# Performance work log

Measured on AMD Instinct MI355X. Metric: run time of the kernel, lower is better.

The kernel has to match this reference:

```python
import jax, jax.numpy as jnp
import numpy as np

N_ATOMS = 100000
N_EDGES = 1000000
HIDDEN = 64
OUT_DIM = 128
N_LAYERS = 3
N_ELEMENTS = 100


def setup_inputs() -> dict:
    key = jax.random.key(0)
    ks = jax.random.split(key, 14)
    s = 0.05
    return {
        "atomic_numbers": jax.random.randint(ks[0], (N_ATOMS,), 0, N_ELEMENTS),
        "positions": jax.random.normal(ks[1], (N_ATOMS, 3), jnp.float32),
        "lattice": jax.random.normal(ks[2], (3, 3), jnp.float32),
        "edge_index": jax.random.randint(ks[3], (2, N_EDGES), 0, N_ATOMS),
        "emb_table": jax.random.normal(ks[4], (N_ELEMENTS, HIDDEN), jnp.float32) * s,
        "W_lin": jax.random.normal(ks[5], (N_LAYERS, HIDDEN, HIDDEN), jnp.float32) * s,
        "b_lin": jax.random.normal(ks[6], (N_LAYERS, HIDDEN), jnp.float32) * s,
        "W_gate": jax.random.normal(ks[7], (N_LAYERS, 2 * HIDDEN, HIDDEN), jnp.float32) * s,
        "b_gate": jax.random.normal(ks[8], (N_LAYERS, HIDDEN), jnp.float32) * s,
        "W_out1": jax.random.normal(ks[9], (HIDDEN, HIDDEN), jnp.float32) * s,
        "b_out1": jax.random.normal(ks[10], (HIDDEN,), jnp.float32) * s,
        "W_out2": jax.random.normal(ks[11], (HIDDEN, OUT_DIM), jnp.float32) * s,
        "b_out2": jax.random.normal(ks[12], (OUT_DIM,), jnp.float32) * s,
    }


def reference(atomic_numbers, positions, lattice, edge_index,
              emb_table, W_lin, b_lin, W_gate, b_gate,
              W_out1, b_out1, W_out2, b_out2):
    # positions/lattice unused when edge_index is provided (matches original).
    x = emb_table[atomic_numbers]            # [N, H] embedding lookup
    row, col = edge_index[0], edge_index[1]
    n = x.shape[0]
    for i in range(W_lin.shape[0]):          # fixed small layer count
        xn = x[col]                          # [E, H] neighbor gather
        gate_in = jnp.concatenate([x[row], xn], axis=-1)  # [E, 2H]
        gate = jax.nn.sigmoid(gate_in @ W_gate[i] + b_gate[i])
        messages = gate * (xn @ W_lin[i] + b_lin[i])       # [E, H]
        agg = jax.ops.segment_sum(messages, row, num_segments=n)  # scatter-add
        x = jax.nn.relu(agg + x @ W_lin[i] + b_lin[i])
    pooled = x.mean(axis=0)                  # [H] mean pool over atoms
    h = jax.nn.relu(pooled @ W_out1 + b_out1)
    return h @ W_out2 + b_out2               # [OUT_DIM]
```

## Files before the change

### kernel.cpp

```cpp
#include <hip/hip_runtime.h>
#include <hip/hip_bf16.h>
#include <stdint.h>


#define H 64
#define SCAN_BS 256
#define SCAN_ELEMS 1024

typedef __attribute__((ext_vector_type(8))) short bf16x8;
typedef __attribute__((ext_vector_type(4))) float f32x4;

__device__ __forceinline__ float sigmoidf_fast(float z) {
  return __builtin_amdgcn_rcpf(1.f + __expf(-z));
}

__device__ __forceinline__ ushort f2bf(float f) {
  uint32_t u = __float_as_uint(f);
  u = (u + 0x7fffu + ((u >> 16) & 1u)) >> 16;
  return (ushort)u;
}
__device__ __forceinline__ uint32_t pack_gl(float gc, float lin) {
  uint32_t ug = __float_as_uint(gc);
  ug = (ug + 0x7fffu + ((ug >> 16) & 1u)) >> 16;
  uint32_t ul = __float_as_uint(lin);
  ul = ((ul + 0x7fffu + ((ul >> 16) & 1u)) >> 16) << 16;
  return ul | ug;
}
__device__ __forceinline__ float unpack_gc(uint32_t p) {
  return __uint_as_float(p << 16);
}
__device__ __forceinline__ float unpack_lin(uint32_t p) {
  return __uint_as_float(p & 0xffff0000u);
}

__global__ void hist_kernel(const int* __restrict__ row, int* __restrict__ hist,
                            int E) {
  for (int e = blockIdx.x * blockDim.x + threadIdx.x; e < E;
       e += gridDim.x * blockDim.x)
    atomicAdd(&hist[row[e]], 1);
}

__global__ __launch_bounds__(SCAN_BS) void scan_partial_kernel(
    const int* __restrict__ hist, int* __restrict__ bsum, int N) {
  __shared__ int red[SCAN_BS];
  const int tid = threadIdx.x;
  const int base = blockIdx.x * SCAN_ELEMS + tid * 4;
  int s = 0;
  if (base + 3 < N) {
    const int4 v = *(const int4*)(hist + base);
    s = v.x + v.y + v.z + v.w;
  } else {
    for (int j = 0; j < 4; j++) if (base + j < N) s += hist[base + j];
  }
  red[tid] = s;
  __syncthreads();
  for (int off = SCAN_BS / 2; off > 0; off >>= 1) {
    if (tid < off) red[tid] += red[tid + off];
    __syncthreads();
  }
  if (tid == 0) bsum[blockIdx.x] = red[0];
}

__global__ __launch_bounds__(1024) void scan_bsum_kernel(
    const int* __restrict__ bsum, int* __restrict__ boff, int nb) {
  __shared__ int sh[1024];
  const int tid = threadIdx.x;
  const int mine = (tid < nb) ? bsum[tid] : 0;
  sh[tid] = mine;
  __syncthreads();
  for (int off = 1; off < 1024; off <<= 1) {
    const int v = (tid >= off) ? sh[tid - off] : 0;
    __syncthreads();
    sh[tid] += v;
    __syncthreads();
  }
  if (tid < nb) boff[tid] = sh[tid] - mine;
}

__global__ __launch_bounds__(SCAN_BS) void scan_apply_kernel(
    const int* __restrict__ hist, const int* __restrict__ boff,
    int* __restrict__ offs, int* __restrict__ offs_work, int N, int E) {
  __shared__ int red[SCAN_BS];
  const int tid = threadIdx.x;
  const int base = blockIdx.x * SCAN_ELEMS + tid * 4;
  int v0 = 0, v1 = 0, v2 = 0, v3 = 0;
  if (base + 3 < N) {
    const int4 v = *(const int4*)(hist + base);
    v0 = v.x; v1 = v.y; v2 = v.z; v3 = v.w;
  } else {
    if (base < N)     v0 = hist[base];
    if (base + 1 < N) v1 = hist[base + 1];
    if (base + 2 < N) v2 = hist[base + 2];
    if (base + 3 < N) v3 = hist[base + 3];
  }
  const int s = v0 + v1 + v2 + v3;
  red[tid] = s;
  __syncthreads();
  for (int off = 1; off < SCAN_BS; off <<= 1) {
    const int v = (tid >= off) ? red[tid - off] : 0;
    __syncthreads();
    red[tid] += v;
    __syncthreads();
  }
  int run = boff[blockIdx.x] + red[tid] - s;
  if (base < N)     { offs[base] = run;     offs_work[base] = run;     run += v0; }
  if (base + 1 < N) { offs[base + 1] = run; offs_work[base + 1] = run; run += v1; }
  if (base + 2 < N) { offs[base + 2] = run; offs_work[base + 2] = run; run += v2; }
  if (base + 3 < N) { offs[base + 3] = run; offs_work[base + 3] = run; run += v3; }
  if (blockIdx.x == 0 && tid == 0) offs[N] = E;
}

__global__ void scatter_kernel(const int* __restrict__ row,
                               const int* __restrict__ col,
                               int* __restrict__ offs_work,
                               int* __restrict__ cols, int E) {
  for (int e = blockIdx.x * blockDim.x + threadIdx.x; e < E;
       e += gridDim.x * blockDim.x) {
    const int pos = atomicAdd(&offs_work[row[e]], 1);
    cols[pos] = col[e];
  }
}

template <bool FIRST>
__global__ __launch_bounds__(256) void node_mm3_mfma(
    const ushort* __restrict__ x, const int* __restrict__ an,
    const float* __restrict__ emb, const float* __restrict__ Wl,
    const float* __restrict__ bl, const float* __restrict__ Wgr,
    const float* __restrict__ Wgc, const float* __restrict__ bg,
    float* __restrict__ gr, uint32_t* __restrict__ glpk, int N) {
  const int tid = threadIdx.x;
  const int lane = tid & 63, wid = tid >> 6;
  const int l15 = lane & 15, kg = lane >> 4;

  bf16x8 bfrag[3][4][2];
#pragma unroll
  for (int mat = 0; mat < 3; mat++) {
    const float* Wm = (mat == 0) ? Wl : (mat == 1) ? Wgr : Wgc;
#pragma unroll
    for (int nt = 0; nt < 4; nt++) {
#pragma unroll
      for (int ks = 0; ks < 2; ks++) {
        const float* wp = Wm + (size_t)(ks * 32 + kg * 8) * H + nt * 16 + l15;
        bf16x8 b;
#pragma unroll
        for (int j = 0; j < 8; j++) b[j] = (short)f2bf(wp[(size_t)j * H]);
        bfrag[mat][nt][ks] = b;
      }
    }
  }

  const int mbase = blockIdx.x * 64 + wid * 16;
  const int arow = mbase + l15;
  const int arow_c = min(arow, N - 1);

  bf16x8 afrag0, afrag1;
  if (FIRST) {
    const int a = an[arow_c];
    const float* src = emb + (size_t)a * H + kg * 8;
    const float4 u0 = *(const float4*)(src);
    const float4 u1 = *(const float4*)(src + 4);
    const float4 u2 = *(const float4*)(src + 32);
    const float4 u3 = *(const float4*)(src + 36);
    bf16x8 t0, t1;
    t0[0] = (short)f2bf(u0.x); t0[1] = (short)f2bf(u0.y);
    t0[2] = (short)f2bf(u0.z); t0[3] = (short)f2bf(u0.w);
    t0[4] = (short)f2bf(u1.x); t0[5] = (short)f2bf(u1.y);
    t0[6] = (short)f2bf(u1.z); t0[7] = (short)f2bf(u1.w);
    t1[0] = (short)f2bf(u2.x); t1[1] = (short)f2bf(u2.y);
    t1[2] = (short)f2bf(u2.z); t1[3] = (short)f2bf(u2.w);
    t1[4] = (short)f2bf(u3.x); t1[5] = (short)f2bf(u3.y);
    t1[6] = (short)f2bf(u3.z); t1[7] = (short)f2bf(u3.w);
    afrag0 = t0; afrag1 = t1;
  } else {
    const ushort* src = x + (size_t)arow_c * H + kg * 8;
    afrag0 = *(const bf16x8*)(src);
    afrag1 = *(const bf16x8*)(src + 32);
  }

  f32x4 accL[4], accR[4], accC[4];
#pragma unroll
  for (int nt = 0; nt < 4; nt++) {
    const float blv = bl[nt * 16 + l15];
    const float bgv = bg[nt * 16 + l15];
    accL[nt] = (f32x4){blv, blv, blv, blv};
    accR[nt] = (f32x4){0.f, 0.f, 0.f, 0.f};
    accC[nt] = (f32x4){bgv, bgv, bgv, bgv};
  }
#pragma unroll
  for (int nt = 0; nt < 4; nt++) {
    accL[nt] = __builtin_amdgcn_mfma_f32_16x16x32_bf16(afrag0, bfrag[0][nt][0], accL[nt], 0, 0, 0);
    accL[nt] = __builtin_amdgcn_mfma_f32_16x16x32_bf16(afrag1, bfrag[0][nt][1], accL[nt], 0, 0, 0);
    accR[nt] = __builtin_amdgcn_mfma_f32_16x16x32_bf16(afrag0, bfrag[1][nt][0], accR[nt], 0, 0, 0);
    accR[nt] = __builtin_amdgcn_mfma_f32_16x16x32_bf16(afrag1, bfrag[1][nt][1], accR[nt], 0, 0, 0);
    accC[nt] = __builtin_amdgcn_mfma_f32_16x16x32_bf16(afrag0, bfrag[2][nt][0], accC[nt], 0, 0, 0);
    accC[nt] = __builtin_amdgcn_mfma_f32_16x16x32_bf16(afrag1, bfrag[2][nt][1], accC[nt], 0, 0, 0);
  }
#pragma unroll
  for (int nt = 0; nt < 4; nt++) {
#pragma unroll
    for (int r = 0; r < 4; r++) {
      const int atom = mbase + kg * 4 + r;
      if (atom < N) {
        const size_t o = (size_t)atom * H + nt * 16 + l15;
        gr[o] = accR[nt][r];
        glpk[o] = pack_gl(accC[nt][r], accL[nt][r]);
      }
    }
  }
}

__global__ __launch_bounds__(256) void agg_kernel(
    const float* __restrict__ gr, const uint32_t* __restrict__ glpk,
    const int* __restrict__ offs, const int* __restrict__ cols,
    ushort* __restrict__ x, int N) {
  const int lane = threadIdx.x & 63, w = threadIdx.x >> 6;
  for (int i = blockIdx.x * 4 + w; i < N; i += gridDim.x * 4) {
    const int s = offs[i], e = offs[i + 1];
    const float gri = gr[(size_t)i * H + lane];
    float acc = 0.f;
    for (int cb = s; cb < e; cb += 64) {
      const int nchunk = min(64, e - cb);
      const int myc = (lane < nchunk) ? cols[cb + lane] : 0;
      int j = 0;
      for (; j + 3 < nchunk; j += 4) {
        const int c0 = __shfl(myc, j + 0), c1 = __shfl(myc, j + 1);
        const int c2 = __shfl(myc, j + 2), c3 = __shfl(myc, j + 3);
        const uint32_t p0 = glpk[(size_t)c0 * H + lane];
        const uint32_t p1 = glpk[(size_t)c1 * H + lane];
        const uint32_t p2 = glpk[(size_t)c2 * H + lane];
        const uint32_t p3 = glpk[(size_t)c3 * H + lane];
        acc += unpack_lin(p0) * sigmoidf_fast(gri + unpack_gc(p0));
        acc += unpack_lin(p1) * sigmoidf_fast(gri + unpack_gc(p1));
        acc += unpack_lin(p2) * sigmoidf_fast(gri + unpack_gc(p2));
        acc += unpack_lin(p3) * sigmoidf_fast(gri + unpack_gc(p3));
      }
      for (; j < nchunk; j++) {
        const int c0 = __shfl(myc, j);
        const uint32_t p0 = glpk[(size_t)c0 * H + lane];
        acc += unpack_lin(p0) * sigmoidf_fast(gri + unpack_gc(p0));
      }
    }
    const float li = unpack_lin(glpk[(size_t)i * H + lane]);
    x[(size_t)i * H + lane] = f2bf(fmaxf(acc + li, 0.f));
  }
}

__global__ void pool_kernel(const ushort* __restrict__ x,
                            float* __restrict__ pool, int N) {
  __shared__ float ps[4][64];
  const int tid = threadIdx.x, c = tid & 63, wid = tid >> 6;
  float s = 0.f;
  for (int i = blockIdx.x * 4 + wid; i < N; i += gridDim.x * 4)
    s += __uint_as_float(((uint32_t)x[(size_t)i * H + c]) << 16);
  ps[wid][c] = s;
  __syncthreads();
  if (tid < 64) {
    const float t = ps[0][tid] + ps[1][tid] + ps[2][tid] + ps[3][tid];
    atomicAdd(&pool[tid], t);
  }
}

__global__ void mlp_kernel(const float* __restrict__ pool,
                           const float* __restrict__ W1,
                           const float* __restrict__ b1,
                           const float* __restrict__ W2,
                           const float* __restrict__ b2,
                           float* __restrict__ out, float invN) {
  __shared__ float p[64], h[64];
  const int tid = threadIdx.x;
  if (tid < 64) p[tid] = pool[tid] * invN;
  __syncthreads();
  if (tid < 64) {
    float s = b1[tid];
    for (int k = 0; k < 64; k++) s = fmaf(p[k], W1[k * 64 + tid], s);
    h[tid] = fmaxf(s, 0.f);
  }
  __syncthreads();
  float s = b2[tid];
  for (int k = 0; k < 64; k++) s = fmaf(h[k], W2[k * 128 + tid], s);
  out[tid] = s;
}

extern "C" void kernel_launch(void* const* d_in, const int* in_sizes, int n_in,
                              void* d_out, int out_size, void* d_ws,
                              size_t ws_size, hipStream_t stream) {
  const int*   an  = (const int*)d_in[0];
  const int*   ei  = (const int*)d_in[3];
  const float* emb = (const float*)d_in[4];
  const float* Wl  = (const float*)d_in[5];
  const float* bl  = (const float*)d_in[6];
  const float* Wg  = (const float*)d_in[7];
  const float* bg  = (const float*)d_in[8];
  const float* W1  = (const float*)d_in[9];
  const float* b1  = (const float*)d_in[10];
  const float* W2  = (const float*)d_in[11];
  const float* b2  = (const float*)d_in[12];
  float* out = (float*)d_out;

  const int N = in_sizes[0];
  const int E = in_sizes[3] / 2;
  const int* row = ei;
  const int* col = ei + E;

  const size_t NH = (size_t)N * H;
  char* ws = (char*)d_ws;
  ushort*   x    = (ushort*)(ws);
  float*    gr   = (float*)(ws + NH * 2);
  uint32_t* glpk = (uint32_t*)(ws + NH * 2 + NH * 4);
  char* p = ws + NH * 2 + NH * 4 + NH * 4;
  int* hist      = (int*)p;  p += ((size_t)N + 1) * 4;
  int* offs      = (int*)p;  p += ((size_t)N + 1) * 4;
  int* offs_work = (int*)p;  p += ((size_t)N + 1) * 4;
  int* cols      = (int*)p;  p += (size_t)E * 4;
  int* bsum      = (int*)p;  p += 4096;
  int* boff      = (int*)p;  p += 4096;
  float* pool    = (float*)p;

  const int nb = (N + SCAN_ELEMS - 1) / SCAN_ELEMS;
  hipMemsetAsync(hist, 0, (size_t)N * 4, stream);
  hist_kernel<<<2048, 256, 0, stream>>>(row, hist, E);
  scan_partial_kernel<<<nb, SCAN_BS, 0, stream>>>(hist, bsum, N);
  scan_bsum_kernel<<<1, 1024, 0, stream>>>(bsum, boff, nb);
  scan_apply_kernel<<<nb, SCAN_BS, 0, stream>>>(hist, boff, offs, offs_work, N, E);
  scatter_kernel<<<2048, 256, 0, stream>>>(row, col, offs_work, cols, E);

  const int mmGrid = (N + 63) / 64;
  const int aggGrid = (N + 3) / 4;
  for (int l = 0; l < 3; l++) {
    const float* Wl_l  = Wl + (size_t)l * H * H;
    const float* bl_l  = bl + (size_t)l * H;
    const float* Wgr_l = Wg + (size_t)l * 2 * H * H;
    const float* Wgc_l = Wgr_l + H * H;
    const float* bg_l  = bg + (size_t)l * H;
    if (l == 0)
      node_mm3_mfma<true><<<mmGrid, 256, 0, stream>>>(
          x, an, emb, Wl_l, bl_l, Wgr_l, Wgc_l, bg_l, gr, glpk, N);
    else
      node_mm3_mfma<false><<<mmGrid, 256, 0, stream>>>(
          x, an, emb, Wl_l, bl_l, Wgr_l, Wgc_l, bg_l, gr, glpk, N);
    agg_kernel<<<aggGrid, 256, 0, stream>>>(gr, glpk, offs, cols, x, N);
  }

  hipMemsetAsync(pool, 0, 64 * sizeof(float), stream);
  pool_kernel<<<1024, 256, 0, stream>>>(x, pool, N);
  mlp_kernel<<<1, 128, 0, stream>>>(pool, W1, b1, W2, b2, out, 1.0f / (float)N);
}
```

Before: 445.1 us.

## Build CSR via two-level bucket sort with LDS-local atomics

Replaces the per-row global histogram, three-kernel scan and global-atomic scatter with a bucketed counting sort. Edges are first binned into buckets of 128 rows using shared-memory histograms and per-block atomic reservations. Each bucket then builds its local CSR offsets and column list in shared memory. This cuts contended global atomics and random scatter writes, in exchange for an extra E*8-byte intermediate edge buffer and a bucket count limited to 1024 (shared arrays sized for it).

```diff
diff --git a/kernel.cpp b/kernel.cpp
--- a/kernel.cpp
+++ b/kernel.cpp
@@ -4,8 +4,8 @@
 
 
 #define H 64
-#define SCAN_BS 256
-#define SCAN_ELEMS 1024
+#define BSHIFT 7
+#define BROWS 128
 
 typedef __attribute__((ext_vector_type(8))) short bf16x8;
 typedef __attribute__((ext_vector_type(4))) float f32x4;
@@ -33,39 +33,25 @@
   return __uint_as_float(p & 0xffff0000u);
 }
 
-__global__ void hist_kernel(const int* __restrict__ row, int* __restrict__ hist,
-                            int E) {
-  for (int e = blockIdx.x * blockDim.x + threadIdx.x; e < E;
-       e += gridDim.x * blockDim.x)
-    atomicAdd(&hist[row[e]], 1);
-}
-
-__global__ __launch_bounds__(SCAN_BS) void scan_partial_kernel(
-    const int* __restrict__ hist, int* __restrict__ bsum, int N) {
-  __shared__ int red[SCAN_BS];
-  const int tid = threadIdx.x;
-  const int base = blockIdx.x * SCAN_ELEMS + tid * 4;
-  int s = 0;
-  if (base + 3 < N) {
-    const int4 v = *(const int4*)(hist + base);
-    s = v.x + v.y + v.z + v.w;
-  } else {
-    for (int j = 0; j < 4; j++) if (base + j < N) s += hist[base + j];
-  }
-  red[tid] = s;
-  __syncthreads();
-  for (int off = SCAN_BS / 2; off > 0; off >>= 1) {
-    if (tid < off) red[tid] += red[tid + off];
-    __syncthreads();
-  }
-  if (tid == 0) bsum[blockIdx.x] = red[0];
-}
-
-__global__ __launch_bounds__(1024) void scan_bsum_kernel(
-    const int* __restrict__ bsum, int* __restrict__ boff, int nb) {
+__global__ __launch_bounds__(256) void bucket_hist_kernel(
+    const int* __restrict__ row, int* __restrict__ bcnt, int E, int nbuck) {
+  __shared__ int cnt[1024];
+  const int tid = threadIdx.x;
+  for (int b = tid; b < nbuck; b += 256) cnt[b] = 0;
+  __syncthreads();
+  for (int e = blockIdx.x * blockDim.x + tid; e < E; e += gridDim.x * blockDim.x)
+    atomicAdd(&cnt[row[e] >> BSHIFT], 1);
+  __syncthreads();
+  for (int b = tid; b < nbuck; b += 256)
+    if (cnt[b]) atomicAdd(&bcnt[b], cnt[b]);
+}
+
+__global__ __launch_bounds__(1024) void bucket_scan_kernel(
+    const int* __restrict__ bcnt, int* __restrict__ bstart,
+    int* __restrict__ bcur, int* __restrict__ offs, int nbuck, int N, int E) {
   __shared__ int sh[1024];
   const int tid = threadIdx.x;
-  const int mine = (tid < nb) ? bsum[tid] : 0;
+  const int mine = (tid < nbuck) ? bcnt[tid] : 0;
   sh[tid] = mine;
   __syncthreads();
   for (int off = 1; off < 1024; off <<= 1) {
@@ -74,50 +60,76 @@
     sh[tid] += v;
     __syncthreads();
   }
-  if (tid < nb) boff[tid] = sh[tid] - mine;
-}
-
-__global__ __launch_bounds__(SCAN_BS) void scan_apply_kernel(
-    const int* __restrict__ hist, const int* __restrict__ boff,
-    int* __restrict__ offs, int* __restrict__ offs_work, int N, int E) {
-  __shared__ int red[SCAN_BS];
-  const int tid = threadIdx.x;
-  const int base = blockIdx.x * SCAN_ELEMS + tid * 4;
-  int v0 = 0, v1 = 0, v2 = 0, v3 = 0;
-  if (base + 3 < N) {
-    const int4 v = *(const int4*)(hist + base);
-    v0 = v.x; v1 = v.y; v2 = v.z; v3 = v.w;
-  } else {
-    if (base < N)     v0 = hist[base];
-    if (base + 1 < N) v1 = hist[base + 1];
-    if (base + 2 < N) v2 = hist[base + 2];
-    if (base + 3 < N) v3 = hist[base + 3];
-  }
-  const int s = v0 + v1 + v2 + v3;
-  red[tid] = s;
-  __syncthreads();
-  for (int off = 1; off < SCAN_BS; off <<= 1) {
-    const int v = (tid >= off) ? red[tid - off] : 0;
+  if (tid < nbuck) {
+    const int ex = sh[tid] - mine;
+    bstart[tid] = ex;
+    bcur[tid] = ex;
+  }
+  if (tid == 0) {
+    bstart[nbuck] = E;
+    offs[N] = E;
+  }
+}
+
+#define SCHUNK 4096
+__global__ __launch_bounds__(256) void bucket_scatter_kernel(
+    const int* __restrict__ row, const int* __restrict__ col,
+    int* __restrict__ bcur, uint2* __restrict__ ebuf, int E, int nbuck) {
+  __shared__ int cnt[1024], base[1024];
+  const int tid = threadIdx.x;
+  const int start = blockIdx.x * SCHUNK;
+  const int end = min(start + SCHUNK, E);
+  for (int b = tid; b < nbuck; b += 256) cnt[b] = 0;
+  __syncthreads();
+  for (int e = start + tid; e < end; e += 256)
+    atomicAdd(&cnt[row[e] >> BSHIFT], 1);
+  __syncthreads();
+  for (int b = tid; b < nbuck; b += 256) {
+    if (cnt[b]) base[b] = atomicAdd(&bcur[b], cnt[b]);
+    cnt[b] = 0;
+  }
+  __syncthreads();
+  for (int e = start + tid; e < end; e += 256) {
+    const int r = row[e];
+    const int b = r >> BSHIFT;
+    const int pos = base[b] + atomicAdd(&cnt[b], 1);
+    ebuf[pos] = make_uint2((uint32_t)r, (uint32_t)col[e]);
+  }
+}
+
+__global__ __launch_bounds__(256) void csr_build_kernel(
+    const uint2* __restrict__ ebuf, const int* __restrict__ bstart,
+    int* __restrict__ offs, int* __restrict__ cols, int N) {
+  __shared__ int cnt[BROWS], sc[BROWS];
+  const int tid = threadIdx.x;
+  const int b = blockIdx.x;
+  const int bs = bstart[b], be = bstart[b + 1];
+  const int rowbase = b << BSHIFT;
+  if (tid < BROWS) cnt[tid] = 0;
+  __syncthreads();
+  for (int e = bs + tid; e < be; e += 256)
+    atomicAdd(&cnt[ebuf[e].x & (BROWS - 1)], 1);
+  __syncthreads();
+  if (tid < BROWS) sc[tid] = cnt[tid];
+  __syncthreads();
+  for (int off = 1; off < BROWS; off <<= 1) {
+    const int v = (tid >= off && tid < BROWS) ? sc[tid - off] : 0;
     __syncthreads();
-    red[tid] += v;
+    if (tid < BROWS) sc[tid] += v;
     __syncthreads();
   }
-  int run = boff[blockIdx.x] + red[tid] - s;
-  if (base < N)     { offs[base] = run;     offs_work[base] = run;     run += v0; }
-  if (base + 1 < N) { offs[base + 1] = run; offs_work[base + 1] = run; run += v1; }
-  if (base + 2 < N) { offs[base + 2] = run; offs_work[base + 2] = run; run += v2; }
-  if (base + 3 < N) { offs[base + 3] = run; offs_work[base + 3] = run; run += v3; }
-  if (blockIdx.x == 0 && tid == 0) offs[N] = E;
-}
-
-__global__ void scatter_kernel(const int* __restrict__ row,
-                               const int* __restrict__ col,
-                               int* __restrict__ offs_work,
-                               int* __restrict__ cols, int E) {
-  for (int e = blockIdx.x * blockDim.x + threadIdx.x; e < E;
-       e += gridDim.x * blockDim.x) {
-    const int pos = atomicAdd(&offs_work[row[e]], 1);
-    cols[pos] = col[e];
+  if (tid < BROWS) {
+    sc[tid] -= cnt[tid];
+    cnt[tid] = 0;
+    const int r = rowbase + tid;
+    if (r < N) offs[r] = bs + sc[tid];
+  }
+  __syncthreads();
+  for (int e = bs + tid; e < be; e += 256) {
+    const uint2 u = ebuf[e];
+    const int rl = u.x & (BROWS - 1);
+    const int pos = sc[rl] + atomicAdd(&cnt[rl], 1);
+    cols[bs + pos] = (int)u.y;
   }
 }
 
@@ -141,10 +153,10 @@
 #pragma unroll
       for (int ks = 0; ks < 2; ks++) {
         const float* wp = Wm + (size_t)(ks * 32 + kg * 8) * H + nt * 16 + l15;
-        bf16x8 b;
-#pragma unroll
-        for (int j = 0; j < 8; j++) b[j] = (short)f2bf(wp[(size_t)j * H]);
-        bfrag[mat][nt][ks] = b;
+        bf16x8 bb;
+#pragma unroll
+        for (int j = 0; j < 8; j++) bb[j] = (short)f2bf(wp[(size_t)j * H]);
+        bfrag[mat][nt][ks] = bb;
       }
     }
   }
@@ -301,6 +313,7 @@
   const int E = in_sizes[3] / 2;
   const int* row = ei;
   const int* col = ei + E;
+  const int nbuck = (N + BROWS - 1) >> BSHIFT;
 
   const size_t NH = (size_t)N * H;
   char* ws = (char*)d_ws;
@@ -308,21 +321,20 @@
   float*    gr   = (float*)(ws + NH * 2);
   uint32_t* glpk = (uint32_t*)(ws + NH * 2 + NH * 4);
   char* p = ws + NH * 2 + NH * 4 + NH * 4;
-  int* hist      = (int*)p;  p += ((size_t)N + 1) * 4;
-  int* offs      = (int*)p;  p += ((size_t)N + 1) * 4;
-  int* offs_work = (int*)p;  p += ((size_t)N + 1) * 4;
-  int* cols      = (int*)p;  p += (size_t)E * 4;
-  int* bsum      = (int*)p;  p += 4096;
-  int* boff      = (int*)p;  p += 4096;
-  float* pool    = (float*)p;
-
-  const int nb = (N + SCAN_ELEMS - 1) / SCAN_ELEMS;
-  hipMemsetAsync(hist, 0, (size_t)N * 4, stream);
-  hist_kernel<<<2048, 256, 0, stream>>>(row, hist, E);
-  scan_partial_kernel<<<nb, SCAN_BS, 0, stream>>>(hist, bsum, N);
-  scan_bsum_kernel<<<1, 1024, 0, stream>>>(bsum, boff, nb);
-  scan_apply_kernel<<<nb, SCAN_BS, 0, stream>>>(hist, boff, offs, offs_work, N, E);
-  scatter_kernel<<<2048, 256, 0, stream>>>(row, col, offs_work, cols, E);
+  int*   offs   = (int*)p;   p += ((size_t)N + 1) * 4;
+  int*   cols   = (int*)p;   p += (size_t)E * 4;
+  int*   bcnt   = (int*)p;   p += 4096;
+  int*   bstart = (int*)p;   p += 4100;
+  int*   bcur   = (int*)p;   p += 4096;
+  uint2* ebuf   = (uint2*)p; p += (size_t)E * 8;
+  float* pool   = (float*)p;
+
+  hipMemsetAsync(bcnt, 0, (size_t)nbuck * 4, stream);
+  bucket_hist_kernel<<<1024, 256, 0, stream>>>(row, bcnt, E, nbuck);
+  bucket_scan_kernel<<<1, 1024, 0, stream>>>(bcnt, bstart, bcur, offs, nbuck, N, E);
+  bucket_scatter_kernel<<<(E + SCHUNK - 1) / SCHUNK, 256, 0, stream>>>(
+      row, col, bcur, ebuf, E, nbuck);
+  csr_build_kernel<<<nbuck, 256, 0, stream>>>(ebuf, bstart, offs, cols, N);
 
   const int mmGrid = (N + 63) / 64;
   const int aggGrid = (N + 3) / 4;
```

Result: faster. 403.7 us (-9.3%).
